# Kernel tuning notes

Hardware: AMD Instinct MI355X
Metric: run time of the kernel (lower is better)

Reference implementation:

```python
import jax, jax.numpy as jnp
import numpy as np

SEQ_LEN = 4096
HIDDEN = 1280
NUM_HEADS = 16
HEAD_DIM = HIDDEN // NUM_HEADS  # 80
NUM_SEQS = 8


def setup_inputs() -> dict:
    key = jax.random.key(0)
    ks = jax.random.split(key, 8)
    x = jax.random.normal(ks[0], (SEQ_LEN, HIDDEN), dtype=jnp.float32)
    # rotary tables: use cos/sin of random angles so they are bounded like real RoPE tables
    ang = jax.random.uniform(ks[1], (SEQ_LEN, HEAD_DIM), dtype=jnp.float32) * 6.283185
    cos = jnp.cos(ang)
    sin = jnp.sin(ang)
    # variable-length packed segments: strictly increasing boundaries incl. 0 and SEQ_LEN
    rng = np.random.default_rng(0)
    inner = np.sort(rng.choice(np.arange(1, SEQ_LEN), size=NUM_SEQS - 1, replace=False))
    cu_seqlens = jnp.asarray(np.concatenate([[0], inner, [SEQ_LEN]]), dtype=jnp.int32)
    s = 0.02
    w_qkv = jax.random.normal(ks[2], (HIDDEN, 3 * HIDDEN), dtype=jnp.float32) * s
    b_qkv = jnp.zeros((3 * HIDDEN,), dtype=jnp.float32)
    w_proj = jax.random.normal(ks[3], (HIDDEN, HIDDEN), dtype=jnp.float32) * s
    b_proj = jnp.zeros((HIDDEN,), dtype=jnp.float32)
    return {"x": x, "cu_seqlens": cu_seqlens, "cos": cos, "sin": sin,
            "w_qkv": w_qkv, "b_qkv": b_qkv, "w_proj": w_proj, "b_proj": b_proj}


def _rotate_half(t):
    d = t.shape[-1] // 2
    return jnp.concatenate([-t[..., d:], t[..., :d]], axis=-1)


def _apply_rope(q, k, cos, sin):
    # q,k: (S,H,D); cos,sin: (S,D) broadcast over heads, computed in fp32
    c = cos[:, None, :].astype(jnp.float32)
    s = sin[:, None, :].astype(jnp.float32)
    qf, kf = q.astype(jnp.float32), k.astype(jnp.float32)
    q_out = qf * c + _rotate_half(qf) * s
    k_out = kf * c + _rotate_half(kf) * s
    return q_out.astype(q.dtype), k_out.astype(k.dtype)


def reference(x, cu_seqlens, cos, sin, w_qkv, b_qkv, w_proj, b_proj):
    S = x.shape[0]
    scale = HEAD_DIM ** (-0.5)
    qkv = (x @ w_qkv + b_qkv).reshape(S, 3, NUM_HEADS, HEAD_DIM)
    q, k, v = qkv[:, 0], qkv[:, 1], qkv[:, 2]  # each (S,H,D)
    q, k = _apply_rope(q, k, cos, sin)
    # block-diagonal varlen attention via segment-id mask (same math as per-chunk softmax)
    pos = jnp.arange(S)
    seg = jnp.searchsorted(cu_seqlens[1:], pos, side='right')  # (S,) segment id
    mask = seg[:, None] == seg[None, :]  # (S,S) block-diagonal
    scores = jnp.einsum('shd,thd->hst', q, k) * scale  # (H,S,S)
    scores = jnp.where(mask[None], scores.astype(jnp.float32), jnp.finfo(jnp.float32).min)
    attn = jax.nn.softmax(scores, axis=-1).astype(q.dtype)
    out = jnp.einsum('hst,thd->shd', attn, v).reshape(S, NUM_HEADS * HEAD_DIM)
    return out @ w_proj + b_proj
```

## Files before the change

kernel.cpp:

```cpp
#include <hip/hip_runtime.h>
#include <cstdint>
#include <cstddef>

typedef __bf16 bf16x8 __attribute__((ext_vector_type(8)));
typedef float f32x4 __attribute__((ext_vector_type(4)));

#define SEQ   4096
#define HID   1280
#define NH    16
#define HD    80

__device__ __forceinline__ unsigned short f2bf(float f) {
  unsigned int u = __float_as_uint(f);
  unsigned int r = u + 0x7FFFu + ((u >> 16) & 1u);
  return (unsigned short)(r >> 16);
}
__device__ __forceinline__ float bf2f(unsigned short h) {
  return __uint_as_float(((unsigned int)h) << 16);
}
__device__ __forceinline__ __bf16 us2bf(unsigned short u) {
  union { unsigned short s; __bf16 b; } c; c.s = u; return c.b;
}
__device__ __forceinline__ void dma16(const void* g, void* l) {
  __builtin_amdgcn_global_load_lds((const __attribute__((address_space(1))) unsigned int*)g,
                                   (__attribute__((address_space(3))) unsigned int*)l, 16, 0, 0);
}

__global__ __launch_bounds__(256) void split_hi_kernel(const float* __restrict__ x,
                                                       unsigned short* __restrict__ hi,
                                                       int n4) {
  int i = blockIdx.x * 256 + threadIdx.x;
  if (i >= n4) return;
  float4 v = *((const float4*)x + i);
  *((ushort4*)hi + i) = make_ushort4(f2bf(v.x), f2bf(v.y), f2bf(v.z), f2bf(v.w));
}

__global__ __launch_bounds__(256) void tsplit_kernel(const float* __restrict__ W,
                                                     unsigned short* __restrict__ Thi,
                                                     unsigned short* __restrict__ Tlo,
                                                     int K, int N) {
  __shared__ float tile[32][33];
  int n0 = blockIdx.x * 32, k0 = blockIdx.y * 32;
  int tx = threadIdx.x & 31, ty = threadIdx.x >> 5;
#pragma unroll
  for (int i = 0; i < 32; i += 8)
    tile[ty + i][tx] = W[(size_t)(k0 + ty + i) * N + n0 + tx];
  __syncthreads();
#pragma unroll
  for (int i = 0; i < 32; i += 8) {
    float v = tile[tx][ty + i];
    size_t idx = (size_t)(n0 + ty + i) * K + (size_t)(k0 + tx);
    unsigned short h = f2bf(v);
    Thi[idx] = h;
    Tlo[idx] = f2bf(v - bf2f(h));
  }
}

__global__ __launch_bounds__(256, 3) void gemm128_x2(
    const unsigned short* __restrict__ A, const unsigned short* __restrict__ Bh,
    const unsigned short* __restrict__ Bl, const float* __restrict__ bias,
    float* __restrict__ out0, float* __restrict__ out1, float* __restrict__ out2,
    int M, int N, int K) {
  __shared__ __align__(16) unsigned short sALL[3 * 8192];

  const int t = threadIdx.x;
  const int lane = t & 63, wave = t >> 6;
  const int c16 = lane & 15, quad = lane >> 4;
  const int bm = blockIdx.y * 128, bn = blockIdx.x * 128;
  const int wr = (wave >> 1) * 64, wc = (wave & 1) * 64;
  const int lrow = lane >> 3;
  const int lswz = (lane & 7) ^ lrow;

  f32x4 acc[4][4];
#pragma unroll
  for (int i = 0; i < 4; ++i)
#pragma unroll
    for (int j = 0; j < 4; ++j) acc[i][j] = (f32x4){0.f, 0.f, 0.f, 0.f};

  const unsigned short* gp[12];
#pragma unroll
  for (int i = 0; i < 12; ++i) {
    const int ua = wave * 12 + i;
    const int arr = ua >> 4, sub = ua & 15;
    const unsigned short* g = (arr == 0) ? A : (arr == 1) ? Bh : Bl;
    const int rowg = ((arr == 0) ? bm : bn) + sub * 8 + lrow;
    gp[i] = g + (size_t)rowg * K + lswz * 8;
  }

  for (int k0 = 0; k0 < K; k0 += 64) {
    __syncthreads();
#pragma unroll
    for (int i = 0; i < 12; ++i)
      dma16(gp[i] + k0, &sALL[(wave * 12 + i) * 512]);
    __syncthreads();
#pragma unroll
    for (int ks = 0; ks < 2; ++ks) {
      bf16x8 a[4], bh[4], bl[4];
#pragma unroll
      for (int mi = 0; mi < 4; ++mi) {
        const int row = wr + mi * 16 + c16;
        const int off = row * 64 + (((ks * 4 + quad) ^ (row & 7)) * 8);
        a[mi] = *(const bf16x8*)&sALL[off];
      }
#pragma unroll
      for (int ni = 0; ni < 4; ++ni) {
        const int row = wc + ni * 16 + c16;
        const int off = row * 64 + (((ks * 4 + quad) ^ (row & 7)) * 8);
        bh[ni] = *(const bf16x8*)&sALL[8192 + off];
        bl[ni] = *(const bf16x8*)&sALL[16384 + off];
      }
#pragma unroll
      for (int mi = 0; mi < 4; ++mi)
#pragma unroll
        for (int ni = 0; ni < 4; ++ni) {
          acc[mi][ni] = __builtin_amdgcn_mfma_f32_16x16x32_bf16(a[mi], bh[ni], acc[mi][ni], 0, 0, 0);
          acc[mi][ni] = __builtin_amdgcn_mfma_f32_16x16x32_bf16(a[mi], bl[ni], acc[mi][ni], 0, 0, 0);
        }
    }
  }
#pragma unroll
  for (int ni = 0; ni < 4; ++ni) {
    int colg = bn + wc + ni * 16 + c16;
    float bv = bias[colg];
    float* op;
    int c = colg;
    if (c < 1280) op = out0;
    else if (c < 2560) { op = out1; c -= 1280; }
    else { op = out2; c -= 2560; }
#pragma unroll
    for (int mi = 0; mi < 4; ++mi)
#pragma unroll
      for (int r = 0; r < 4; ++r) {
        int rowg = bm + wr + mi * 16 + quad * 4 + r;
        op[(size_t)rowg * 1280 + c] = acc[mi][ni][r] + bv;
      }
  }
}

__global__ __launch_bounds__(256) void rope_pack_kernel(
    float* __restrict__ qf, const float* __restrict__ kf,
    const float* __restrict__ cs, const float* __restrict__ sn,
    unsigned short* __restrict__ khi, unsigned short* __restrict__ klo) {
  const int h = blockIdx.y;
  const int s = blockIdx.x * 64 + (threadIdx.x >> 2);
  const int p = threadIdx.x & 3;
  float* qrow = qf + (size_t)s * HID + h * HD;
  const float* krow = kf + (size_t)s * HID + h * HD;
  const float* cr = cs + (size_t)s * HD;
  const float* sr = sn + (size_t)s * HD;
  unsigned short* kh = khi + ((size_t)h * SEQ + s) * HD;
  unsigned short* kl = klo + ((size_t)h * SEQ + s) * HD;
#pragma unroll
  for (int j = 0; j < 10; ++j) {
    int d = 10 * p + j;
    float c0 = cr[d], s0 = sr[d], c1 = cr[d + 40], s1 = sr[d + 40];
    float q0 = qrow[d], q1 = qrow[d + 40];
    qrow[d]      = q0 * c0 - q1 * s0;
    qrow[d + 40] = q1 * c1 + q0 * s1;
    float k0 = krow[d], k1 = krow[d + 40];
    float kn0 = k0 * c0 - k1 * s0;
    float kn1 = k1 * c1 + k0 * s1;
    unsigned short h0 = f2bf(kn0), h1 = f2bf(kn1);
    kh[d] = h0;      kl[d] = f2bf(kn0 - bf2f(h0));
    kh[d + 40] = h1; kl[d + 40] = f2bf(kn1 - bf2f(h1));
  }
}

__global__ __launch_bounds__(256) void vt_pack_kernel(const float* __restrict__ vf,
                                                      unsigned short* __restrict__ vthi,
                                                      unsigned short* __restrict__ vtlo,
                                                      unsigned int* __restrict__ ctr) {
  if (blockIdx.x == 0 && blockIdx.y == 0 && threadIdx.x == 0) *ctr = 0u;
  __shared__ unsigned short sTh[80][72];
  __shared__ unsigned short sTl[80][72];
  const int h = blockIdx.y;
  const int s0 = blockIdx.x * 64;
  const int t = threadIdx.x;
  {
    int row = t >> 2, p = (t & 3) * 20;
    const float* src = vf + (size_t)(s0 + row) * HID + h * HD + p;
#pragma unroll
    for (int i = 0; i < 5; ++i) {
      float4 v = *(const float4*)(src + 4 * i);
      float vv[4] = {v.x, v.y, v.z, v.w};
#pragma unroll
      for (int j = 0; j < 4; ++j) {
        int d = p + 4 * i + j;
        unsigned short hu = f2bf(vv[j]);
        sTh[d][row] = hu;
        sTl[d][row] = f2bf(vv[j] - bf2f(hu));
      }
    }
  }
  __syncthreads();
  if (t < 160) {
    int d = t >> 1, half = (t & 1) * 32;
    size_t base = (size_t)(h * HD + d) * SEQ + s0 + half;
#pragma unroll
    for (int i = 0; i < 8; ++i) {
      *(ushort4*)&vthi[base + 4 * i] = *(ushort4*)&sTh[d][half + 4 * i];
      *(ushort4*)&vtlo[base + 4 * i] = *(ushort4*)&sTl[d][half + 4 * i];
    }
  }
}

__global__ __launch_bounds__(256, 3) void attn_kernel(
    const float* __restrict__ qf, const unsigned short* __restrict__ khi,
    const unsigned short* __restrict__ klo, const unsigned short* __restrict__ vthi,
    const unsigned short* __restrict__ vtlo, const int* __restrict__ cu,
    unsigned short* __restrict__ ohi, unsigned int* __restrict__ ctr) {
  __shared__ __align__(16) unsigned short sKh[5120], sKl[5120];
  __shared__ __align__(16) unsigned short sVh[5120], sVl[5120];
  __shared__ int cu_s[9];
  __shared__ unsigned int s_u;

  const int t = threadIdx.x;
  const int lane = t & 63, wave = t >> 6;
  const int c16 = lane & 15, quad = lane >> 4;
  const int lr8 = lane >> 3;
  const int vswz = (lane & 7) ^ lr8;
  const int addrA = ((((2 * quad) & 3) * 16) + c16) << 2;
  const int addrB = ((((2 * quad + 1) & 3) * 16) + c16) << 2;

  if (t < 9) cu_s[t] = cu[t];

  for (;;) {
    __syncthreads();
    if (t == 0) s_u = atomicAdd(ctr, 1u);
    __syncthreads();
    const unsigned int u = s_u;
    if (u >= 1024u) break;
    const int h = (int)(u >> 6);
    const int r0 = (int)(u & 63u) * 64;

    const int q_my = r0 + wave * 16 + c16;
    int sq = 0, sg0 = 0, sg1 = 0;
#pragma unroll
    for (int i = 1; i < 8; ++i) {
      sq  += (q_my    >= cu_s[i]) ? 1 : 0;
      sg0 += (r0      >= cu_s[i]) ? 1 : 0;
      sg1 += (r0 + 63 >= cu_s[i]) ? 1 : 0;
    }
    const int kb_lo = cu_s[sq], kb_hi = cu_s[sq + 1];
    const int ck0 = cu_s[sg0] & ~63;
    const int kend = cu_s[sg1 + 1];
    const int nchunk = (kend - ck0 + 63) >> 6;

    const float qsc = 0.11180339887498949f;
    bf16x8 qh[3], ql[3];
    {
      const float* qrow = qf + (size_t)q_my * HID + h * HD;
#pragma unroll
      for (int ks = 0; ks < 3; ++ks) {
        const int d = ks * 32 + quad * 8;
        bf16x8 hf = {}, lf = {};
        if (d < 80) {
          float4 v0 = *(const float4*)(qrow + d);
          float4 v1 = *(const float4*)(qrow + d + 4);
          float vv[8] = {v0.x, v0.y, v0.z, v0.w, v1.x, v1.y, v1.z, v1.w};
#pragma unroll
          for (int j = 0; j < 8; ++j) {
            float v = vv[j] * qsc;
            unsigned short hu = f2bf(v);
            hf[j] = us2bf(hu);
            lf[j] = us2bf(f2bf(v - bf2f(hu)));
          }
        }
        qh[ks] = hf; ql[ks] = lf;
      }
    }

    f32x4 O[5];
#pragma unroll
    for (int dt = 0; dt < 5; ++dt) O[dt] = (f32x4){0.f, 0.f, 0.f, 0.f};
    float m_i = -1e30f, l_i = 0.f;

    {
      const unsigned short* gk = (wave & 2) ? klo : khi;
      unsigned short* lk = ((wave & 2) ? sKl : sKh) + (wave & 1) * 2560;
      const size_t kb = ((size_t)h * SEQ + ck0) * 80 + (size_t)(wave & 1) * 2560 + lane * 8;
#pragma unroll
      for (int i2 = 0; i2 < 5; ++i2) dma16(gk + kb + i2 * 512, lk + i2 * 512);
      const unsigned short* gv = (wave & 2) ? vtlo : vthi;
      unsigned short* lv = (wave & 2) ? sVl : sVh;
      const int u0 = (wave & 1) * 5;
#pragma unroll
      for (int i2 = 0; i2 < 5; ++i2) {
        const int uu = u0 + i2;
        dma16(gv + (size_t)(h * HD + 8 * uu + lr8) * SEQ + ck0 + vswz * 8, lv + uu * 512);
      }
    }
    __syncthreads();

    for (int ci = 0; ci < nchunk; ++ci) {
      const int ck = ck0 + ci * 64;
      f32x4 sc[4];
#pragma unroll
      for (int nt = 0; nt < 4; ++nt) sc[nt] = (f32x4){0.f, 0.f, 0.f, 0.f};
#pragma unroll
      for (int nt = 0; nt < 4; ++nt) {
        const int krow = nt * 16 + c16;
#pragma unroll
        for (int ks = 0; ks < 3; ++ks) {
          const int d = ks * 32 + quad * 8;
          bf16x8 kh = {}, kl = {};
          if (d < 80) {
            kh = *(const bf16x8*)&sKh[krow * 80 + d];
            kl = *(const bf16x8*)&sKl[krow * 80 + d];
          }
          sc[nt] = __builtin_amdgcn_mfma_f32_16x16x32_bf16(kh, qh[ks], sc[nt], 0, 0, 0);
          sc[nt] = __builtin_amdgcn_mfma_f32_16x16x32_bf16(kh, ql[ks], sc[nt], 0, 0, 0);
          sc[nt] = __builtin_amdgcn_mfma_f32_16x16x32_bf16(kl, qh[ks], sc[nt], 0, 0, 0);
        }
      }
      float mx = -1e30f;
#pragma unroll
      for (int nt = 0; nt < 4; ++nt)
#pragma unroll
        for (int r = 0; r < 4; ++r) {
          const int kg = ck + nt * 16 + quad * 4 + r;
          const bool ok = (kg >= kb_lo) && (kg < kb_hi);
          float v = ok ? sc[nt][r] : -1e30f;
          sc[nt][r] = v;
          mx = fmaxf(mx, v);
        }
      mx = fmaxf(mx, __shfl_xor(mx, 16));
      mx = fmaxf(mx, __shfl_xor(mx, 32));
      const float mnew = fmaxf(m_i, mx);
      const float alpha = __expf(m_i - mnew);
      float ps = 0.f;
      unsigned int pk[4][4];
#pragma unroll
      for (int nt = 0; nt < 4; ++nt)
#pragma unroll
        for (int r = 0; r < 4; ++r) {
          const float s = sc[nt][r];
          const float p = (s > -1e29f) ? __expf(s - mnew) : 0.f;
          ps += p;
          const unsigned int pu = __float_as_uint(p);
          const unsigned short ph = (unsigned short)(pu >> 16);
          const unsigned short pl = f2bf(p - bf2f(ph));
          pk[nt][r] = (unsigned int)ph | ((unsigned int)pl << 16);
        }
      ps += __shfl_xor(ps, 16);
      ps += __shfl_xor(ps, 32);
      l_i = l_i * alpha + ps;
      m_i = mnew;
      float aR[4];
#pragma unroll
      for (int r = 0; r < 4; ++r)
        aR[r] = __uint_as_float((unsigned)__builtin_amdgcn_ds_bpermute(
                    (quad * 4 + r) << 2, __float_as_int(alpha)));
#pragma unroll
      for (int dt = 0; dt < 5; ++dt) {
        f32x4 o = O[dt];
        o[0] *= aR[0]; o[1] *= aR[1]; o[2] *= aR[2]; o[3] *= aR[3];
        O[dt] = o;
      }
      __syncthreads();
      if (ci + 1 < nchunk) {
        const unsigned short* gk = (wave & 2) ? klo : khi;
        unsigned short* lk = ((wave & 2) ? sKl : sKh) + (wave & 1) * 2560;
        const size_t kb = ((size_t)h * SEQ + ck + 64) * 80 + (size_t)(wave & 1) * 2560 + lane * 8;
#pragma unroll
        for (int i2 = 0; i2 < 5; ++i2) dma16(gk + kb + i2 * 512, lk + i2 * 512);
      }
#pragma unroll
      for (int ks = 0; ks < 2; ++ks) {
        unsigned int vj[8];
#pragma unroll
        for (int j = 0; j < 8; ++j) {
          const int addr = (j < 4) ? addrA : addrB;
          const int r = j & 3;
          const int v0 = __builtin_amdgcn_ds_bpermute(addr, (int)pk[2 * ks + 0][r]);
          const int v1 = __builtin_amdgcn_ds_bpermute(addr, (int)pk[2 * ks + 1][r]);
          vj[j] = (unsigned int)((quad & 2) ? v1 : v0);
        }
        union { unsigned int w[4]; bf16x8 v; } ph, pl;
        ph.w[0] = __builtin_amdgcn_perm(vj[1], vj[0], 0x05040100u);
        ph.w[1] = __builtin_amdgcn_perm(vj[3], vj[2], 0x05040100u);
        ph.w[2] = __builtin_amdgcn_perm(vj[5], vj[4], 0x05040100u);
        ph.w[3] = __builtin_amdgcn_perm(vj[7], vj[6], 0x05040100u);
        pl.w[0] = __builtin_amdgcn_perm(vj[1], vj[0], 0x07060302u);
        pl.w[1] = __builtin_amdgcn_perm(vj[3], vj[2], 0x07060302u);
        pl.w[2] = __builtin_amdgcn_perm(vj[5], vj[4], 0x07060302u);
        pl.w[3] = __builtin_amdgcn_perm(vj[7], vj[6], 0x07060302u);
        const int g = ks * 4 + quad;
#pragma unroll
        for (int dt = 0; dt < 5; ++dt) {
          const int d = dt * 16 + c16;
          const int off = d * 64 + ((g ^ (d & 7)) * 8);
          bf16x8 vh = *(const bf16x8*)&sVh[off];
          bf16x8 vl = *(const bf16x8*)&sVl[off];
          O[dt] = __builtin_amdgcn_mfma_f32_16x16x32_bf16(ph.v, vh, O[dt], 0, 0, 0);
          O[dt] = __builtin_amdgcn_mfma_f32_16x16x32_bf16(ph.v, vl, O[dt], 0, 0, 0);
          O[dt] = __builtin_amdgcn_mfma_f32_16x16x32_bf16(pl.v, vh, O[dt], 0, 0, 0);
        }
      }
      __syncthreads();
      if (ci + 1 < nchunk) {
        const unsigned short* gv = (wave & 2) ? vtlo : vthi;
        unsigned short* lv = (wave & 2) ? sVl : sVh;
        const int u0 = (wave & 1) * 5;
#pragma unroll
        for (int i2 = 0; i2 < 5; ++i2) {
          const int uu = u0 + i2;
          dma16(gv + (size_t)(h * HD + 8 * uu + lr8) * SEQ + (ck + 64) + vswz * 8, lv + uu * 512);
        }
      }
    }
    const float inv = 1.0f / l_i;
    float iR[4];
#pragma unroll
    for (int r = 0; r < 4; ++r)
      iR[r] = __uint_as_float((unsigned)__builtin_amdgcn_ds_bpermute(
                  (quad * 4 + r) << 2, __float_as_int(inv)));
#pragma unroll
    for (int dt = 0; dt < 5; ++dt)
#pragma unroll
      for (int r = 0; r < 4; ++r) {
        const int rowg = r0 + wave * 16 + quad * 4 + r;
        ohi[(size_t)rowg * HID + h * HD + dt * 16 + c16] = f2bf(O[dt][r] * iR[r]);
      }
  }
}

extern "C" void kernel_launch(void* const* d_in, const int* in_sizes, int n_in,
                              void* d_out, int out_size, void* d_ws, size_t ws_size,
                              hipStream_t stream) {
  const float* x      = (const float*)d_in[0];
  const int*   cu     = (const int*)d_in[1];
  const float* cs     = (const float*)d_in[2];
  const float* sn     = (const float*)d_in[3];
  const float* w_qkv  = (const float*)d_in[4];
  const float* b_qkv  = (const float*)d_in[5];
  const float* w_proj = (const float*)d_in[6];
  const float* b_proj = (const float*)d_in[7];
  float* out = (float*)d_out;

  char* ws = (char*)d_ws;
  float*          qf     = (float*)(ws + 0);
  float*          kf     = (float*)(ws + 20971520ULL);
  unsigned short* vthi   = (unsigned short*)(ws + 20971520ULL);
  unsigned short* vtlo   = (unsigned short*)(ws + 31457280ULL);
  float*          vf     = (float*)(ws + 41943040ULL);
  unsigned short* o_hi   = (unsigned short*)(ws + 41943040ULL);
  unsigned short* x_hi   = (unsigned short*)(ws + 62914560ULL);
  unsigned short* khi    = (unsigned short*)(ws + 62914560ULL);
  unsigned short* klo    = (unsigned short*)(ws + 73400320ULL);
  unsigned short* wqt_hi = (unsigned short*)(ws + 83886080ULL);
  unsigned short* wqt_lo = (unsigned short*)(ws + 93716480ULL);
  unsigned short* wpt_hi = (unsigned short*)(ws + 103546880ULL);
  unsigned short* wpt_lo = (unsigned short*)(ws + 106823680ULL);
  unsigned int*   ctr    = (unsigned int*)(ws + 83886080ULL);

  split_hi_kernel<<<5120, 256, 0, stream>>>(x, x_hi, 1310720);
  tsplit_kernel<<<dim3(120, 40), 256, 0, stream>>>(w_qkv, wqt_hi, wqt_lo, 1280, 3840);
  tsplit_kernel<<<dim3(40, 40), 256, 0, stream>>>(w_proj, wpt_hi, wpt_lo, 1280, 1280);
  gemm128_x2<<<dim3(30, 32), 256, 0, stream>>>(x_hi, wqt_hi, wqt_lo, b_qkv,
                                               qf, kf, vf, 4096, 3840, 1280);
  rope_pack_kernel<<<dim3(64, 16), 256, 0, stream>>>(qf, kf, cs, sn, khi, klo);
  vt_pack_kernel<<<dim3(64, 16), 256, 0, stream>>>(vf, vthi, vtlo, ctr);
  attn_kernel<<<768, 256, 0, stream>>>(qf, khi, klo, vthi, vtlo, cu, o_hi, ctr);
  gemm128_x2<<<dim3(10, 32), 256, 0, stream>>>(o_hi, wpt_hi, wpt_lo, b_proj,
                                               out, nullptr, nullptr, 4096, 1280, 1280);
}
```

Before: 401.7 us.

## Double-buffer K/V, process two query tiles per wave, static grid

The attention kernel now gives each wave two 16-row query tiles (128 rows per block), so each K/V chunk staged in LDS is reused twice. K and V are double-buffered, so the next chunk's DMA overlaps compute and the number of barriers per chunk drops. The persistent atomic work queue is replaced by a static 512-block grid with a head-interleaved block order, and s_setprio is raised around the MFMA sections. In exchange, register and LDS pressure rise (occupancy hint lowered from 3 to 2 blocks), and segment-straddling blocks may now iterate over more chunks.

```diff
diff --git a/kernel.cpp b/kernel.cpp
--- a/kernel.cpp
+++ b/kernel.cpp
@@ -204,15 +204,69 @@
   }
 }
 
-__global__ __launch_bounds__(256, 3) void attn_kernel(
+
+#define SMAX(SC, MI, LI, PK, AR, KBLO, KBHI)                                   \
+  do {                                                                         \
+    float mx = -1e30f;                                                         \
+    _Pragma("unroll") for (int nt = 0; nt < 4; ++nt)                           \
+        _Pragma("unroll") for (int r = 0; r < 4; ++r) {                        \
+      const int kg = ck + nt * 16 + quad * 4 + r;                              \
+      const bool ok = (kg >= (KBLO)) && (kg < (KBHI));                         \
+      float v = ok ? SC[nt][r] : -1e30f;                                       \
+      SC[nt][r] = v;                                                           \
+      mx = fmaxf(mx, v);                                                       \
+    }                                                                          \
+    mx = fmaxf(mx, __shfl_xor(mx, 16));                                        \
+    mx = fmaxf(mx, __shfl_xor(mx, 32));                                        \
+    const float mnew = fmaxf(MI, mx);                                          \
+    const float alpha = __expf(MI - mnew);                                     \
+    float ps = 0.f;                                                            \
+    _Pragma("unroll") for (int nt = 0; nt < 4; ++nt)                           \
+        _Pragma("unroll") for (int r = 0; r < 4; ++r) {                        \
+      const float s = SC[nt][r];                                               \
+      const float p = (s > -1e29f) ? __expf(s - mnew) : 0.f;                   \
+      ps += p;                                                                 \
+      const unsigned int pu = __float_as_uint(p);                              \
+      const unsigned short ph_ = (unsigned short)(pu >> 16);                   \
+      const unsigned short pl_ = f2bf(p - bf2f(ph_));                          \
+      PK[nt][r] = (unsigned int)ph_ | ((unsigned int)pl_ << 16);               \
+    }                                                                          \
+    ps += __shfl_xor(ps, 16);                                                  \
+    ps += __shfl_xor(ps, 32);                                                  \
+    LI = LI * alpha + ps;                                                      \
+    MI = mnew;                                                                 \
+    _Pragma("unroll") for (int r = 0; r < 4; ++r)                              \
+        AR[r] = __uint_as_float((unsigned)__builtin_amdgcn_ds_bpermute(        \
+            (quad * 4 + r) << 2, __float_as_int(alpha)));                      \
+  } while (0)
+
+#define BUILD_P(PK, PHU, PLU)                                                  \
+  do {                                                                         \
+    unsigned int vj[8];                                                        \
+    _Pragma("unroll") for (int j = 0; j < 8; ++j) {                            \
+      const int addr = (j < 4) ? addrA : addrB;                                \
+      const int r = j & 3;                                                     \
+      const int v0 = __builtin_amdgcn_ds_bpermute(addr, (int)PK[2 * ks + 0][r]); \
+      const int v1 = __builtin_amdgcn_ds_bpermute(addr, (int)PK[2 * ks + 1][r]); \
+      vj[j] = (unsigned int)((quad & 2) ? v1 : v0);                            \
+    }                                                                          \
+    PHU.w[0] = __builtin_amdgcn_perm(vj[1], vj[0], 0x05040100u);               \
+    PHU.w[1] = __builtin_amdgcn_perm(vj[3], vj[2], 0x05040100u);               \
+    PHU.w[2] = __builtin_amdgcn_perm(vj[5], vj[4], 0x05040100u);               \
+    PHU.w[3] = __builtin_amdgcn_perm(vj[7], vj[6], 0x05040100u);               \
+    PLU.w[0] = __builtin_amdgcn_perm(vj[1], vj[0], 0x07060302u);               \
+    PLU.w[1] = __builtin_amdgcn_perm(vj[3], vj[2], 0x07060302u);               \
+    PLU.w[2] = __builtin_amdgcn_perm(vj[5], vj[4], 0x07060302u);               \
+    PLU.w[3] = __builtin_amdgcn_perm(vj[7], vj[6], 0x07060302u);               \
+  } while (0)
+
+__global__ __launch_bounds__(256, 2) void attn_kernel(
     const float* __restrict__ qf, const unsigned short* __restrict__ khi,
     const unsigned short* __restrict__ klo, const unsigned short* __restrict__ vthi,
     const unsigned short* __restrict__ vtlo, const int* __restrict__ cu,
-    unsigned short* __restrict__ ohi, unsigned int* __restrict__ ctr) {
-  __shared__ __align__(16) unsigned short sKh[5120], sKl[5120];
-  __shared__ __align__(16) unsigned short sVh[5120], sVl[5120];
-  __shared__ int cu_s[9];
-  __shared__ unsigned int s_u;
+    unsigned short* __restrict__ ohi) {
+  __shared__ __align__(16) unsigned short sKh[2][5120], sKl[2][5120];
+  __shared__ __align__(16) unsigned short sVh[2][5120], sVl[2][5120];
 
   const int t = threadIdx.x;
   const int lane = t & 63, wave = t >> 6;
@@ -222,207 +276,177 @@
   const int addrA = ((((2 * quad) & 3) * 16) + c16) << 2;
   const int addrB = ((((2 * quad + 1) & 3) * 16) + c16) << 2;
 
-  if (t < 9) cu_s[t] = cu[t];
-
-  for (;;) {
+  const unsigned int u = (blockIdx.x & 7) * 64 + (blockIdx.x >> 3);
+  const int h = (int)(u >> 5);
+  const int r0 = (int)(u & 31u) * 128;
+
+  int cu_r[9];
+#pragma unroll
+  for (int i = 0; i < 9; ++i) cu_r[i] = cu[i];
+
+  const int q0 = r0 + wave * 16 + c16;
+  const int q1 = q0 + 64;
+  int sq0 = 0, sq1 = 0, sg0 = 0, sg1 = 0;
+#pragma unroll
+  for (int i = 1; i < 8; ++i) {
+    sq0 += (q0 >= cu_r[i]) ? 1 : 0;
+    sq1 += (q1 >= cu_r[i]) ? 1 : 0;
+    sg0 += (r0 >= cu_r[i]) ? 1 : 0;
+    sg1 += (r0 + 127 >= cu_r[i]) ? 1 : 0;
+  }
+  const int kb_lo0 = cu_r[sq0], kb_hi0 = cu_r[sq0 + 1];
+  const int kb_lo1 = cu_r[sq1], kb_hi1 = cu_r[sq1 + 1];
+  const int ck0 = cu_r[sg0] & ~63;
+  const int kend = cu_r[sg1 + 1];
+  const int nchunk = (kend - ck0 + 63) >> 6;
+
+  const float qsc = 0.11180339887498949f;
+  bf16x8 qh0[3], ql0[3], qh1[3], ql1[3];
+  {
+    const float* qrowA = qf + (size_t)q0 * HID + h * HD;
+    const float* qrowB = qf + (size_t)q1 * HID + h * HD;
+#pragma unroll
+    for (int ks = 0; ks < 3; ++ks) {
+      const int d = ks * 32 + quad * 8;
+      bf16x8 hA = {}, lA = {}, hB = {}, lB = {};
+      if (d < 80) {
+        float4 a0 = *(const float4*)(qrowA + d);
+        float4 a1 = *(const float4*)(qrowA + d + 4);
+        float4 b0 = *(const float4*)(qrowB + d);
+        float4 b1 = *(const float4*)(qrowB + d + 4);
+        float va[8] = {a0.x, a0.y, a0.z, a0.w, a1.x, a1.y, a1.z, a1.w};
+        float vb[8] = {b0.x, b0.y, b0.z, b0.w, b1.x, b1.y, b1.z, b1.w};
+#pragma unroll
+        for (int j = 0; j < 8; ++j) {
+          float v = va[j] * qsc;
+          unsigned short hu = f2bf(v);
+          hA[j] = us2bf(hu); lA[j] = us2bf(f2bf(v - bf2f(hu)));
+          v = vb[j] * qsc;
+          hu = f2bf(v);
+          hB[j] = us2bf(hu); lB[j] = us2bf(f2bf(v - bf2f(hu)));
+        }
+      }
+      qh0[ks] = hA; ql0[ks] = lA; qh1[ks] = hB; ql1[ks] = lB;
+    }
+  }
+
+  f32x4 O0[5], O1[5];
+#pragma unroll
+  for (int dt = 0; dt < 5; ++dt) {
+    O0[dt] = (f32x4){0.f, 0.f, 0.f, 0.f};
+    O1[dt] = (f32x4){0.f, 0.f, 0.f, 0.f};
+  }
+  float m0 = -1e30f, l0v = 0.f, m1 = -1e30f, l1v = 0.f;
+
+  auto STAGE = [&](int buf, int ck) {
+    const unsigned short* gk = (wave & 2) ? klo : khi;
+    unsigned short* lk = ((wave & 2) ? sKl[buf] : sKh[buf]) + (wave & 1) * 2560;
+    const size_t kb = ((size_t)h * SEQ + ck) * 80 + (size_t)(wave & 1) * 2560 + lane * 8;
+#pragma unroll
+    for (int i2 = 0; i2 < 5; ++i2) dma16(gk + kb + i2 * 512, lk + i2 * 512);
+    const unsigned short* gv = (wave & 2) ? vtlo : vthi;
+    unsigned short* lv = (wave & 2) ? sVl[buf] : sVh[buf];
+    const int half5 = (wave & 1) * 5;
+#pragma unroll
+    for (int i2 = 0; i2 < 5; ++i2) {
+      const int uu = half5 + i2;
+      dma16(gv + (size_t)(h * HD + 8 * uu + lr8) * SEQ + ck + vswz * 8, lv + uu * 512);
+    }
+  };
+
+  STAGE(0, ck0);
+  int cur = 0;
+
+  for (int ci = 0; ci < nchunk; ++ci) {
+    const int ck = ck0 + ci * 64;
     __syncthreads();
-    if (t == 0) s_u = atomicAdd(ctr, 1u);
-    __syncthreads();
-    const unsigned int u = s_u;
-    if (u >= 1024u) break;
-    const int h = (int)(u >> 6);
-    const int r0 = (int)(u & 63u) * 64;
-
-    const int q_my = r0 + wave * 16 + c16;
-    int sq = 0, sg0 = 0, sg1 = 0;
-#pragma unroll
-    for (int i = 1; i < 8; ++i) {
-      sq  += (q_my    >= cu_s[i]) ? 1 : 0;
-      sg0 += (r0      >= cu_s[i]) ? 1 : 0;
-      sg1 += (r0 + 63 >= cu_s[i]) ? 1 : 0;
-    }
-    const int kb_lo = cu_s[sq], kb_hi = cu_s[sq + 1];
-    const int ck0 = cu_s[sg0] & ~63;
-    const int kend = cu_s[sg1 + 1];
-    const int nchunk = (kend - ck0 + 63) >> 6;
-
-    const float qsc = 0.11180339887498949f;
-    bf16x8 qh[3], ql[3];
-    {
-      const float* qrow = qf + (size_t)q_my * HID + h * HD;
+    if (ci + 1 < nchunk) STAGE(cur ^ 1, ck + 64);
+
+    f32x4 sc0[4], sc1[4];
+#pragma unroll
+    for (int nt = 0; nt < 4; ++nt) {
+      sc0[nt] = (f32x4){0.f, 0.f, 0.f, 0.f};
+      sc1[nt] = (f32x4){0.f, 0.f, 0.f, 0.f};
+    }
+    __builtin_amdgcn_s_setprio(1);
+#pragma unroll
+    for (int nt = 0; nt < 4; ++nt) {
+      const int krow = nt * 16 + c16;
 #pragma unroll
       for (int ks = 0; ks < 3; ++ks) {
         const int d = ks * 32 + quad * 8;
-        bf16x8 hf = {}, lf = {};
+        bf16x8 kh = {}, kl = {};
         if (d < 80) {
-          float4 v0 = *(const float4*)(qrow + d);
-          float4 v1 = *(const float4*)(qrow + d + 4);
-          float vv[8] = {v0.x, v0.y, v0.z, v0.w, v1.x, v1.y, v1.z, v1.w};
-#pragma unroll
-          for (int j = 0; j < 8; ++j) {
-            float v = vv[j] * qsc;
-            unsigned short hu = f2bf(v);
-            hf[j] = us2bf(hu);
-            lf[j] = us2bf(f2bf(v - bf2f(hu)));
-          }
+          kh = *(const bf16x8*)&sKh[cur][krow * 80 + d];
+          kl = *(const bf16x8*)&sKl[cur][krow * 80 + d];
         }
-        qh[ks] = hf; ql[ks] = lf;
-      }
-    }
-
-    f32x4 O[5];
-#pragma unroll
-    for (int dt = 0; dt < 5; ++dt) O[dt] = (f32x4){0.f, 0.f, 0.f, 0.f};
-    float m_i = -1e30f, l_i = 0.f;
-
-    {
-      const unsigned short* gk = (wave & 2) ? klo : khi;
-      unsigned short* lk = ((wave & 2) ? sKl : sKh) + (wave & 1) * 2560;
-      const size_t kb = ((size_t)h * SEQ + ck0) * 80 + (size_t)(wave & 1) * 2560 + lane * 8;
-#pragma unroll
-      for (int i2 = 0; i2 < 5; ++i2) dma16(gk + kb + i2 * 512, lk + i2 * 512);
-      const unsigned short* gv = (wave & 2) ? vtlo : vthi;
-      unsigned short* lv = (wave & 2) ? sVl : sVh;
-      const int u0 = (wave & 1) * 5;
-#pragma unroll
-      for (int i2 = 0; i2 < 5; ++i2) {
-        const int uu = u0 + i2;
-        dma16(gv + (size_t)(h * HD + 8 * uu + lr8) * SEQ + ck0 + vswz * 8, lv + uu * 512);
-      }
-    }
-    __syncthreads();
-
-    for (int ci = 0; ci < nchunk; ++ci) {
-      const int ck = ck0 + ci * 64;
-      f32x4 sc[4];
-#pragma unroll
-      for (int nt = 0; nt < 4; ++nt) sc[nt] = (f32x4){0.f, 0.f, 0.f, 0.f};
-#pragma unroll
-      for (int nt = 0; nt < 4; ++nt) {
-        const int krow = nt * 16 + c16;
-#pragma unroll
-        for (int ks = 0; ks < 3; ++ks) {
-          const int d = ks * 32 + quad * 8;
-          bf16x8 kh = {}, kl = {};
-          if (d < 80) {
-            kh = *(const bf16x8*)&sKh[krow * 80 + d];
-            kl = *(const bf16x8*)&sKl[krow * 80 + d];
-          }
-          sc[nt] = __builtin_amdgcn_mfma_f32_16x16x32_bf16(kh, qh[ks], sc[nt], 0, 0, 0);
-          sc[nt] = __builtin_amdgcn_mfma_f32_16x16x32_bf16(kh, ql[ks], sc[nt], 0, 0, 0);
-          sc[nt] = __builtin_amdgcn_mfma_f32_16x16x32_bf16(kl, qh[ks], sc[nt], 0, 0, 0);
-        }
-      }
-      float mx = -1e30f;
-#pragma unroll
-      for (int nt = 0; nt < 4; ++nt)
-#pragma unroll
-        for (int r = 0; r < 4; ++r) {
-          const int kg = ck + nt * 16 + quad * 4 + r;
-          const bool ok = (kg >= kb_lo) && (kg < kb_hi);
-          float v = ok ? sc[nt][r] : -1e30f;
-          sc[nt][r] = v;
-          mx = fmaxf(mx, v);
-        }
-      mx = fmaxf(mx, __shfl_xor(mx, 16));
-      mx = fmaxf(mx, __shfl_xor(mx, 32));
-      const float mnew = fmaxf(m_i, mx);
-      const float alpha = __expf(m_i - mnew);
-      float ps = 0.f;
-      unsigned int pk[4][4];
-#pragma unroll
-      for (int nt = 0; nt < 4; ++nt)
-#pragma unroll
-        for (int r = 0; r < 4; ++r) {
-          const float s = sc[nt][r];
-          const float p = (s > -1e29f) ? __expf(s - mnew) : 0.f;
-          ps += p;
-          const unsigned int pu = __float_as_uint(p);
-          const unsigned short ph = (unsigned short)(pu >> 16);
-          const unsigned short pl = f2bf(p - bf2f(ph));
-          pk[nt][r] = (unsigned int)ph | ((unsigned int)pl << 16);
-        }
-      ps += __shfl_xor(ps, 16);
-      ps += __shfl_xor(ps, 32);
-      l_i = l_i * alpha + ps;
-      m_i = mnew;
-      float aR[4];
-#pragma unroll
-      for (int r = 0; r < 4; ++r)
-        aR[r] = __uint_as_float((unsigned)__builtin_amdgcn_ds_bpermute(
-                    (quad * 4 + r) << 2, __float_as_int(alpha)));
+        sc0[nt] = __builtin_amdgcn_mfma_f32_16x16x32_bf16(kh, qh0[ks], sc0[nt], 0, 0, 0);
+        sc0[nt] = __builtin_amdgcn_mfma_f32_16x16x32_bf16(kh, ql0[ks], sc0[nt], 0, 0, 0);
+        sc0[nt] = __builtin_amdgcn_mfma_f32_16x16x32_bf16(kl, qh0[ks], sc0[nt], 0, 0, 0);
+        sc1[nt] = __builtin_amdgcn_mfma_f32_16x16x32_bf16(kh, qh1[ks], sc1[nt], 0, 0, 0);
+        sc1[nt] = __builtin_amdgcn_mfma_f32_16x16x32_bf16(kh, ql1[ks], sc1[nt], 0, 0, 0);
+        sc1[nt] = __builtin_amdgcn_mfma_f32_16x16x32_bf16(kl, qh1[ks], sc1[nt], 0, 0, 0);
+      }
+    }
+    __builtin_amdgcn_s_setprio(0);
+
+    unsigned int pk0[4][4], pk1[4][4];
+    float aR0[4], aR1[4];
+    SMAX(sc0, m0, l0v, pk0, aR0, kb_lo0, kb_hi0);
+    SMAX(sc1, m1, l1v, pk1, aR1, kb_lo1, kb_hi1);
+#pragma unroll
+    for (int dt = 0; dt < 5; ++dt) {
+      f32x4 o = O0[dt];
+      o[0] *= aR0[0]; o[1] *= aR0[1]; o[2] *= aR0[2]; o[3] *= aR0[3];
+      O0[dt] = o;
+      o = O1[dt];
+      o[0] *= aR1[0]; o[1] *= aR1[1]; o[2] *= aR1[2]; o[3] *= aR1[3];
+      O1[dt] = o;
+    }
+
+#pragma unroll
+    for (int ks = 0; ks < 2; ++ks) {
+      union { unsigned int w[4]; bf16x8 v; } ph0u, pl0u, ph1u, pl1u;
+      BUILD_P(pk0, ph0u, pl0u);
+      BUILD_P(pk1, ph1u, pl1u);
+      const int g = ks * 4 + quad;
+      __builtin_amdgcn_s_setprio(1);
 #pragma unroll
       for (int dt = 0; dt < 5; ++dt) {
-        f32x4 o = O[dt];
-        o[0] *= aR[0]; o[1] *= aR[1]; o[2] *= aR[2]; o[3] *= aR[3];
-        O[dt] = o;
-      }
-      __syncthreads();
-      if (ci + 1 < nchunk) {
-        const unsigned short* gk = (wave & 2) ? klo : khi;
-        unsigned short* lk = ((wave & 2) ? sKl : sKh) + (wave & 1) * 2560;
-        const size_t kb = ((size_t)h * SEQ + ck + 64) * 80 + (size_t)(wave & 1) * 2560 + lane * 8;
-#pragma unroll
-        for (int i2 = 0; i2 < 5; ++i2) dma16(gk + kb + i2 * 512, lk + i2 * 512);
-      }
-#pragma unroll
-      for (int ks = 0; ks < 2; ++ks) {
-        unsigned int vj[8];
-#pragma unroll
-        for (int j = 0; j < 8; ++j) {
-          const int addr = (j < 4) ? addrA : addrB;
-          const int r = j & 3;
-          const int v0 = __builtin_amdgcn_ds_bpermute(addr, (int)pk[2 * ks + 0][r]);
-          const int v1 = __builtin_amdgcn_ds_bpermute(addr, (int)pk[2 * ks + 1][r]);
-          vj[j] = (unsigned int)((quad & 2) ? v1 : v0);
-        }
-        union { unsigned int w[4]; bf16x8 v; } ph, pl;
-        ph.w[0] = __builtin_amdgcn_perm(vj[1], vj[0], 0x05040100u);
-        ph.w[1] = __builtin_amdgcn_perm(vj[3], vj[2], 0x05040100u);
-        ph.w[2] = __builtin_amdgcn_perm(vj[5], vj[4], 0x05040100u);
-        ph.w[3] = __builtin_amdgcn_perm(vj[7], vj[6], 0x05040100u);
-        pl.w[0] = __builtin_amdgcn_perm(vj[1], vj[0], 0x07060302u);
-        pl.w[1] = __builtin_amdgcn_perm(vj[3], vj[2], 0x07060302u);
-        pl.w[2] = __builtin_amdgcn_perm(vj[5], vj[4], 0x07060302u);
-        pl.w[3] = __builtin_amdgcn_perm(vj[7], vj[6], 0x07060302u);
-        const int g = ks * 4 + quad;
-#pragma unroll
-        for (int dt = 0; dt < 5; ++dt) {
-          const int d = dt * 16 + c16;
-          const int off = d * 64 + ((g ^ (d & 7)) * 8);
-          bf16x8 vh = *(const bf16x8*)&sVh[off];
-          bf16x8 vl = *(const bf16x8*)&sVl[off];
-          O[dt] = __builtin_amdgcn_mfma_f32_16x16x32_bf16(ph.v, vh, O[dt], 0, 0, 0);
-          O[dt] = __builtin_amdgcn_mfma_f32_16x16x32_bf16(ph.v, vl, O[dt], 0, 0, 0);
-          O[dt] = __builtin_amdgcn_mfma_f32_16x16x32_bf16(pl.v, vh, O[dt], 0, 0, 0);
-        }
-      }
-      __syncthreads();
-      if (ci + 1 < nchunk) {
-        const unsigned short* gv = (wave & 2) ? vtlo : vthi;
-        unsigned short* lv = (wave & 2) ? sVl : sVh;
-        const int u0 = (wave & 1) * 5;
-#pragma unroll
-        for (int i2 = 0; i2 < 5; ++i2) {
-          const int uu = u0 + i2;
-          dma16(gv + (size_t)(h * HD + 8 * uu + lr8) * SEQ + (ck + 64) + vswz * 8, lv + uu * 512);
-        }
-      }
-    }
-    const float inv = 1.0f / l_i;
-    float iR[4];
-#pragma unroll
-    for (int r = 0; r < 4; ++r)
-      iR[r] = __uint_as_float((unsigned)__builtin_amdgcn_ds_bpermute(
-                  (quad * 4 + r) << 2, __float_as_int(inv)));
-#pragma unroll
-    for (int dt = 0; dt < 5; ++dt)
-#pragma unroll
-      for (int r = 0; r < 4; ++r) {
-        const int rowg = r0 + wave * 16 + quad * 4 + r;
-        ohi[(size_t)rowg * HID + h * HD + dt * 16 + c16] = f2bf(O[dt][r] * iR[r]);
-      }
-  }
+        const int d = dt * 16 + c16;
+        const int off = d * 64 + ((g ^ (d & 7)) * 8);
+        bf16x8 vh = *(const bf16x8*)&sVh[cur][off];
+        bf16x8 vl = *(const bf16x8*)&sVl[cur][off];
+        O0[dt] = __builtin_amdgcn_mfma_f32_16x16x32_bf16(ph0u.v, vh, O0[dt], 0, 0, 0);
+        O0[dt] = __builtin_amdgcn_mfma_f32_16x16x32_bf16(ph0u.v, vl, O0[dt], 0, 0, 0);
+        O0[dt] = __builtin_amdgcn_mfma_f32_16x16x32_bf16(pl0u.v, vh, O0[dt], 0, 0, 0);
+        O1[dt] = __builtin_amdgcn_mfma_f32_16x16x32_bf16(ph1u.v, vh, O1[dt], 0, 0, 0);
+        O1[dt] = __builtin_amdgcn_mfma_f32_16x16x32_bf16(ph1u.v, vl, O1[dt], 0, 0, 0);
+        O1[dt] = __builtin_amdgcn_mfma_f32_16x16x32_bf16(pl1u.v, vh, O1[dt], 0, 0, 0);
+      }
+      __builtin_amdgcn_s_setprio(0);
+    }
+    cur ^= 1;
+  }
+
+  const float inv0 = 1.0f / l0v;
+  const float inv1 = 1.0f / l1v;
+  float iR0[4], iR1[4];
+#pragma unroll
+  for (int r = 0; r < 4; ++r) {
+    iR0[r] = __uint_as_float((unsigned)__builtin_amdgcn_ds_bpermute(
+                 (quad * 4 + r) << 2, __float_as_int(inv0)));
+    iR1[r] = __uint_as_float((unsigned)__builtin_amdgcn_ds_bpermute(
+                 (quad * 4 + r) << 2, __float_as_int(inv1)));
+  }
+#pragma unroll
+  for (int dt = 0; dt < 5; ++dt)
+#pragma unroll
+    for (int r = 0; r < 4; ++r) {
+      const int row0 = r0 + wave * 16 + quad * 4 + r;
+      ohi[(size_t)row0 * HID + h * HD + dt * 16 + c16] = f2bf(O0[dt][r] * iR0[r]);
+      ohi[(size_t)(row0 + 64) * HID + h * HD + dt * 16 + c16] = f2bf(O1[dt][r] * iR1[r]);
+    }
 }
 
 extern "C" void kernel_launch(void* const* d_in, const int* in_sizes, int n_in,
@@ -461,7 +485,7 @@
                                                qf, kf, vf, 4096, 3840, 1280);
   rope_pack_kernel<<<dim3(64, 16), 256, 0, stream>>>(qf, kf, cs, sn, khi, klo);
   vt_pack_kernel<<<dim3(64, 16), 256, 0, stream>>>(vf, vthi, vtlo, ctr);
-  attn_kernel<<<768, 256, 0, stream>>>(qf, khi, klo, vthi, vtlo, cu, o_hi, ctr);
+  attn_kernel<<<512, 256, 0, stream>>>(qf, khi, klo, vthi, vtlo, cu, o_hi);
   gemm128_x2<<<dim3(10, 32), 256, 0, stream>>>(o_hi, wpt_hi, wpt_lo, b_proj,
                                                out, nullptr, nullptr, 4096, 1280, 1280);
 }
```

Measured after the change: 410.4 us. 2.1% more time.
